# Kernel optimization log

Hardware: AMD Instinct MI355X
Metric: run time of the kernel (lower is better)

The kernel has to match this reference:

```python
import jax, jax.numpy as jnp
import numpy as np

D_MODEL = 512
NUM_HEADS = 8
DEPTH = D_MODEL // NUM_HEADS


def setup_inputs() -> dict:
    key = jax.random.key(0)
    ks = jax.random.split(key, 12)
    B, S, D = 2, 4096, D_MODEL
    scale = 1.0 / np.sqrt(D)
    return {
        "q": jax.random.normal(ks[0], (B, S, D), jnp.float32),
        "k": jax.random.normal(ks[1], (B, S, D), jnp.float32),
        "v": jax.random.normal(ks[2], (B, S, D), jnp.float32),
        "mask": jnp.zeros((B, 1, 1, S), jnp.float32),
        "wq": jax.random.normal(ks[3], (D, D), jnp.float32) * scale,
        "bq": jnp.zeros((D,), jnp.float32),
        "wk": jax.random.normal(ks[4], (D, D), jnp.float32) * scale,
        "bk": jnp.zeros((D,), jnp.float32),
        "wv": jax.random.normal(ks[5], (D, D), jnp.float32) * scale,
        "bv": jnp.zeros((D,), jnp.float32),
        "wo": jax.random.normal(ks[6], (D, D), jnp.float32) * scale,
        "bo": jnp.zeros((D,), jnp.float32),
    }


def _split_heads(x):
    # [B, S, D] -> [B, H, S, depth]
    B, S, _ = x.shape
    return x.reshape(B, S, NUM_HEADS, DEPTH).transpose(0, 2, 1, 3)


def reference(q, k, v, mask, wq, bq, wk, bk, wv, bv, wo, bo):
    B, S, D = q.shape
    query = _split_heads(q @ wq + bq)   # [B,H,S,d]
    key = _split_heads(k @ wk + bk)
    value = _split_heads(v @ wv + bv)
    # NOTE: original module does NOT scale by 1/sqrt(depth)
    score = jnp.einsum("bhqd,bhkd->bhqk", query, key)
    score = score + mask * -1e9
    attn = jax.nn.softmax(score, axis=-1)
    out = jnp.einsum("bhqk,bhkd->bhqd", attn, value)  # [B,H,S,d]
    out = out.transpose(0, 2, 1, 3).reshape(B, S, D)
    return out @ wo + bo
```

## Files before the change

kernel.cpp:

```cpp
#include <hip/hip_runtime.h>

#define NH   8
#define DH   64
#define NB   2
#define SEQ  4096
#define DM   512
#define MR   (NB * SEQ)
#define LSTR 72
#define LOG2E 1.44269504089f
#define NSPL 2
#define KVS  (SEQ / NSPL)
#define RH   (NB * NH * SEQ)
#define PSTR 36

using f16x8 = __attribute__((ext_vector_type(8))) _Float16;
using f32x4 = __attribute__((ext_vector_type(4))) float;
using h2    = __attribute__((ext_vector_type(2))) _Float16;
#define MFMA16(a, b, c) __builtin_amdgcn_mfma_f32_16x16x32_f16(a, b, c, 0, 0, 0)

#if defined(__has_builtin) && __has_builtin(__builtin_amdgcn_exp2f)
#define EXP2(x) __builtin_amdgcn_exp2f(x)
#else
extern "C" __device__ float __ocml_native_exp2_f32(float);
#define EXP2(x) __ocml_native_exp2_f32(x)
#endif

__device__ __forceinline__ unsigned pk_f16(float a, float b) {
    typedef __fp16 fp16v2 __attribute__((ext_vector_type(2)));
    union { fp16v2 h; unsigned u; } c;
    c.h = __builtin_amdgcn_cvt_pkrtz(a, b);
    return c.u;
}
__device__ __forceinline__ float m3(float a, float b, float c) {
    return fmaxf(fmaxf(a, b), c);
}
__device__ __forceinline__ float dot2acc(unsigned u, float c) {
#if defined(__has_builtin) && __has_builtin(__builtin_amdgcn_fdot2)
    h2 a = __builtin_bit_cast(h2, u);
    h2 one = {(_Float16)1.f, (_Float16)1.f};
    return __builtin_amdgcn_fdot2(a, one, c, false);
#else
    h2 a = __builtin_bit_cast(h2, u);
    return c + (float)a[0] + (float)a[1];
#endif
}
__device__ __forceinline__ void async16(void* lds, const void* g) {
    __builtin_amdgcn_global_load_lds(
        (__attribute__((address_space(1))) void*)g,
        (__attribute__((address_space(3))) void*)lds, 16, 0, 0);
}

__global__ __launch_bounds__(256) void cvt_w(
    const float* __restrict__ w0, const float* __restrict__ w1,
    const float* __restrict__ w2, const float* __restrict__ w3,
    _Float16* __restrict__ Wt)
{
    __shared__ _Float16 T[64 * LSTR];
    const int z = blockIdx.z;
    const float* W = (z == 0) ? w0 : (z == 1 ? w1 : (z == 2 ? w2 : w3));
    _Float16* out = Wt + (size_t)z * DM * DM;
    const int t = threadIdx.x;
    const int k0 = blockIdx.x * 64, n0 = blockIdx.y * 64;
#pragma unroll
    for (int i = 0; i < 4; ++i) {
        const int kl  = i * 16 + (t >> 4);
        const int nl4 = (t & 15) * 4;
        float4 u = *(const float4*)(W + (size_t)(k0 + kl) * DM + n0 + nl4);
        T[(nl4 + 0) * LSTR + kl] = (_Float16)u.x;
        T[(nl4 + 1) * LSTR + kl] = (_Float16)u.y;
        T[(nl4 + 2) * LSTR + kl] = (_Float16)u.z;
        T[(nl4 + 3) * LSTR + kl] = (_Float16)u.w;
    }
    __syncthreads();
#pragma unroll
    for (int i = 0; i < 2; ++i) {
        const int nl = i * 32 + (t >> 3);
        const int kc = (t & 7) * 8;
        *(uint4*)(out + (size_t)(n0 + nl) * DM + k0 + kc) = *(const uint4*)&T[nl * LSTR + kc];
    }
}

__global__ __launch_bounds__(256) void maskprep(const float* __restrict__ mask,
                                                float* __restrict__ mw)
{
    const int i = blockIdx.x * 256 + threadIdx.x;
    mw[i] = mask[i] * (-1e9f * LOG2E);
}

__global__ __launch_bounds__(256) void cvt_qkv(
    const float* __restrict__ q, const float* __restrict__ k,
    const float* __restrict__ v,
    _Float16* __restrict__ Qo, _Float16* __restrict__ Ko, _Float16* __restrict__ Vo)
{
    const size_t PER = (size_t)MR * DM;
    size_t base = ((size_t)blockIdx.x * 256 + threadIdx.x) * 8;
    const int tz = (int)(base / PER);
    const size_t off = base % PER;
    const float* s = (tz == 0) ? q : (tz == 1 ? k : v);
    _Float16* d    = (tz == 0) ? Qo : (tz == 1 ? Ko : Vo);
    float4 a = *(const float4*)(s + off);
    float4 b = *(const float4*)(s + off + 4);
    uint4 p = make_uint4(pk_f16(a.x, a.y), pk_f16(a.z, a.w),
                         pk_f16(b.x, b.y), pk_f16(b.z, b.w));
    *(uint4*)(d + off) = p;
}

__global__ __launch_bounds__(256) void proj3(
    const _Float16* __restrict__ Qin, const _Float16* __restrict__ Kin,
    const _Float16* __restrict__ Vin, const _Float16* __restrict__ Wt,
    const float* __restrict__ bq, const float* __restrict__ bk,
    const float* __restrict__ bv,
    _Float16* __restrict__ Qo, _Float16* __restrict__ Ko,
    _Float16* __restrict__ VTo)
{
    __shared__ _Float16 Xs[2][128 * 64];
    __shared__ _Float16 Ws[2][64 * 64];

    const int z = blockIdx.z;
    const _Float16* X = (z == 0) ? Qin : (z == 1 ? Kin : Vin);
    const _Float16* W = Wt + (size_t)z * DM * DM;
    const float* bias = (z == 0) ? bq : (z == 1 ? bk : bv);
    const float scale = (z == 0) ? LOG2E : 1.0f;

    const int t = threadIdx.x;
    const int l = t & 63, w = t >> 6;
    const int m = l & 15, g = l >> 4;
    const int ms = m & 7;
    const int row0 = blockIdx.x * 128;
    const int col0 = blockIdx.y * 64;

    int xr[4], xsw[4];
#pragma unroll
    for (int i = 0; i < 4; ++i) {
        const int c = w * 256 + i * 64 + l;
        xr[i]  = c >> 3;
        xsw[i] = ((c & 7) ^ (xr[i] & 7)) * 8;
    }
    int wr[2], wsw[2];
#pragma unroll
    for (int i = 0; i < 2; ++i) {
        const int c = w * 128 + i * 64 + l;
        wr[i]  = c >> 3;
        wsw[i] = ((c & 7) ^ (wr[i] & 7)) * 8;
    }

#pragma unroll
    for (int i = 0; i < 4; ++i)
        async16(&Xs[0][(w * 256 + i * 64) * 8], X + (size_t)(row0 + xr[i]) * DM + xsw[i]);
#pragma unroll
    for (int i = 0; i < 2; ++i)
        async16(&Ws[0][(w * 128 + i * 64) * 8], W + (size_t)(col0 + wr[i]) * DM + wsw[i]);

    f32x4 acc[2][4] = {};

    for (int k0 = 0; k0 < DM; k0 += 64) {
        const int p = (k0 >> 6) & 1;
        __syncthreads();
        if (k0 + 64 < DM) {
            const int kn = k0 + 64;
#pragma unroll
            for (int i = 0; i < 4; ++i)
                async16(&Xs[p ^ 1][(w * 256 + i * 64) * 8],
                        X + (size_t)(row0 + xr[i]) * DM + kn + xsw[i]);
#pragma unroll
            for (int i = 0; i < 2; ++i)
                async16(&Ws[p ^ 1][(w * 128 + i * 64) * 8],
                        W + (size_t)(col0 + wr[i]) * DM + kn + wsw[i]);
        }
#pragma unroll
        for (int kk = 0; kk < 2; ++kk) {
            const int slot = ((kk * 4 + g) ^ ms) * 8;
            f16x8 a0 = *(const f16x8*)&Xs[p][(w * 32 + m) * 64 + slot];
            f16x8 a1 = *(const f16x8*)&Xs[p][(w * 32 + 16 + m) * 64 + slot];
#pragma unroll
            for (int ct = 0; ct < 4; ++ct) {
                f16x8 bf = *(const f16x8*)&Ws[p][(ct * 16 + m) * 64 + slot];
                acc[0][ct] = MFMA16(a0, bf, acc[0][ct]);
                acc[1][ct] = MFMA16(a1, bf, acc[1][ct]);
            }
        }
    }

    float bv4[4];
#pragma unroll
    for (int ct = 0; ct < 4; ++ct) bv4[ct] = bias[col0 + ct * 16 + m];

    if (z == 2) {
        __syncthreads();
        _Float16* T = &Xs[0][0];
#pragma unroll
        for (int rt = 0; rt < 2; ++rt)
#pragma unroll
            for (int reg = 0; reg < 4; ++reg) {
                const int s_l = w * 32 + rt * 16 + g * 4 + reg;
#pragma unroll
                for (int ct = 0; ct < 4; ++ct) {
                    const int d = ct * 16 + m;
                    T[d * 136 + s_l] = (_Float16)(acc[rt][ct][reg] + bv4[ct]);
                }
            }
        __syncthreads();
        const int bb = row0 >> 12;
        const int s0 = row0 & (SEQ - 1);
#pragma unroll
        for (int j = 0; j < 4; ++j) {
            const int c = j * 256 + t;
            const int d = c >> 4;
            const int sc = (c & 15) * 8;
            *(uint4*)(VTo + (((size_t)bb * NH + blockIdx.y) * DH + d) * SEQ + s0 + sc) =
                *(const uint4*)&T[d * 136 + sc];
        }
    } else {
        _Float16* out = (z == 0) ? Qo : Ko;
#pragma unroll
        for (int rt = 0; rt < 2; ++rt)
#pragma unroll
            for (int reg = 0; reg < 4; ++reg) {
                const int row = row0 + w * 32 + rt * 16 + g * 4 + reg;
                const int bb = row >> 12;
                const int s  = row & (SEQ - 1);
#pragma unroll
                for (int ct = 0; ct < 4; ++ct)
                    out[(((size_t)bb * NH + blockIdx.y) * SEQ + s) * DH + ct * 16 + m] =
                        (_Float16)(scale * (acc[rt][ct][reg] + bv4[ct]));
            }
    }
}

__global__ __launch_bounds__(256) void gemm_out(const _Float16* __restrict__ X,
                                                const _Float16* __restrict__ W,
                                                const float* __restrict__ bias,
                                                float* __restrict__ out)
{
    __shared__ _Float16 Xs[2][128 * 64];
    __shared__ _Float16 Ws[2][64 * 64];

    const int t = threadIdx.x;
    const int l = t & 63, w = t >> 6;
    const int m = l & 15, g = l >> 4;
    const int ms = m & 7;
    const int row0 = blockIdx.x * 128;
    const int col0 = blockIdx.y * 64;

    int xr[4], xsw[4];
#pragma unroll
    for (int i = 0; i < 4; ++i) {
        const int c = w * 256 + i * 64 + l;
        xr[i]  = c >> 3;
        xsw[i] = ((c & 7) ^ (xr[i] & 7)) * 8;
    }
    int wr[2], wsw[2];
#pragma unroll
    for (int i = 0; i < 2; ++i) {
        const int c = w * 128 + i * 64 + l;
        wr[i]  = c >> 3;
        wsw[i] = ((c & 7) ^ (wr[i] & 7)) * 8;
    }

#pragma unroll
    for (int i = 0; i < 4; ++i)
        async16(&Xs[0][(w * 256 + i * 64) * 8], X + (size_t)(row0 + xr[i]) * DM + xsw[i]);
#pragma unroll
    for (int i = 0; i < 2; ++i)
        async16(&Ws[0][(w * 128 + i * 64) * 8], W + (size_t)(col0 + wr[i]) * DM + wsw[i]);

    f32x4 acc[2][4] = {};

    for (int k0 = 0; k0 < DM; k0 += 64) {
        const int p = (k0 >> 6) & 1;
        __syncthreads();
        if (k0 + 64 < DM) {
            const int kn = k0 + 64;
#pragma unroll
            for (int i = 0; i < 4; ++i)
                async16(&Xs[p ^ 1][(w * 256 + i * 64) * 8],
                        X + (size_t)(row0 + xr[i]) * DM + kn + xsw[i]);
#pragma unroll
            for (int i = 0; i < 2; ++i)
                async16(&Ws[p ^ 1][(w * 128 + i * 64) * 8],
                        W + (size_t)(col0 + wr[i]) * DM + kn + wsw[i]);
        }
#pragma unroll
        for (int kk = 0; kk < 2; ++kk) {
            const int slot = ((kk * 4 + g) ^ ms) * 8;
            f16x8 a0 = *(const f16x8*)&Xs[p][(w * 32 + m) * 64 + slot];
            f16x8 a1 = *(const f16x8*)&Xs[p][(w * 32 + 16 + m) * 64 + slot];
#pragma unroll
            for (int ct = 0; ct < 4; ++ct) {
                f16x8 bf = *(const f16x8*)&Ws[p][(ct * 16 + m) * 64 + slot];
                acc[0][ct] = MFMA16(a0, bf, acc[0][ct]);
                acc[1][ct] = MFMA16(a1, bf, acc[1][ct]);
            }
        }
    }

    float bv4[4];
#pragma unroll
    for (int ct = 0; ct < 4; ++ct) bv4[ct] = bias[col0 + ct * 16 + m];

#pragma unroll
    for (int rt = 0; rt < 2; ++rt)
#pragma unroll
        for (int reg = 0; reg < 4; ++reg) {
            const int row = row0 + w * 32 + rt * 16 + g * 4 + reg;
#pragma unroll
            for (int ct = 0; ct < 4; ++ct)
                out[(size_t)row * DM + col0 + ct * 16 + m] = acc[rt][ct][reg] + bv4[ct];
        }
}

__global__ __launch_bounds__(256, 3) void flash_mfma(
    const _Float16* __restrict__ Q, const _Float16* __restrict__ K,
    const _Float16* __restrict__ VT, const float* __restrict__ mw,
    _Float16* __restrict__ Op, float* __restrict__ Ml)
{
    __shared__ _Float16 Ks [2][64 * 64];
    __shared__ _Float16 VTs[2][64 * 64];
    __shared__ unsigned Ps[4][32 * PSTR];

    const int t = threadIdx.x;
    const int l = t & 63, w = t >> 6;
    const int m = l & 15, g = l >> 4;

    const unsigned wfl = blockIdx.x + 32u * blockIdx.y + 512u * blockIdx.z;
    const unsigned o   = (wfl & 7u) * 128u + (wfl >> 3);
    const int q0 = (int)(o & 31u) * 128;
    const int bh = (int)(o >> 5) & 15;
    const int z  = (int)(o >> 9);
    const int b  = bh >> 3;
    const int kb0 = z * KVS;

    const _Float16* Qh  = Q  + (size_t)bh * SEQ * DH;
    const _Float16* Kh  = K  + (size_t)bh * SEQ * DH;
    const _Float16* VTh = VT + (size_t)bh * DH * SEQ;
    const float* mwb = mw + (size_t)b * SEQ;

    const int c0 = w * 128 + l, c1 = c0 + 64;
    const int r0 = c0 >> 3,     r1 = c1 >> 3;
    const int cl0 = (c0 & 7) ^ (r0 & 7), cl1 = (c1 & 7) ^ (r1 & 7);
    const int    gK0 = r0 * DH + cl0 * 8, gK1 = r1 * DH + cl1 * 8;
    const size_t gV0 = (size_t)r0 * SEQ + cl0 * 8, gV1 = (size_t)r1 * SEQ + cl1 * 8;
    const int ldsA = w * 1024, ldsB = ldsA + 512;

    async16(&Ks[0][ldsA], Kh + (size_t)kb0 * DH + gK0);
    async16(&Ks[0][ldsB], Kh + (size_t)kb0 * DH + gK1);
    async16(&VTs[0][ldsA], VTh + kb0 + gV0);
    async16(&VTs[0][ldsB], VTh + kb0 + gV1);

    f16x8 qf[2][2];
#pragma unroll
    for (int h = 0; h < 2; ++h)
#pragma unroll
        for (int kk = 0; kk < 2; ++kk)
            qf[h][kk] = *(const f16x8*)(Qh + (size_t)(q0 + w * 32 + h * 16 + m) * DH +
                                        kk * 32 + g * 8);

    f32x4 mv[4];
#pragma unroll
    for (int kt = 0; kt < 4; ++kt)
        mv[kt] = *(const f32x4*)&mwb[kb0 + kt * 16 + g * 4];

    float m_r[2] = {-INFINITY, -INFINITY}, l_r[2] = {0.f, 0.f};
    f32x4 oacc[2][4] = {};

    unsigned* Pw = &Ps[w][0];
    const int ms = m & 7;

    for (int it = 0; it < KVS / 64; ++it) {
        const int t0 = kb0 + it * 64;
        const int p  = it & 1;
        const bool more = (it + 1 < KVS / 64);
        __syncthreads();

        f32x4 mvn[4];
        if (more) {
            const int tn = t0 + 64;
            async16(&Ks[p ^ 1][ldsA], Kh + (size_t)tn * DH + gK0);
            async16(&Ks[p ^ 1][ldsB], Kh + (size_t)tn * DH + gK1);
            async16(&VTs[p ^ 1][ldsA], VTh + tn + gV0);
            async16(&VTs[p ^ 1][ldsB], VTh + tn + gV1);
#pragma unroll
            for (int kt = 0; kt < 4; ++kt)
                mvn[kt] = *(const f32x4*)&mwb[tn + kt * 16 + g * 4];
        }

        f32x4 sacc[2][4];
#pragma unroll
        for (int kt = 0; kt < 4; ++kt) {
            sacc[0][kt] = mv[kt];
            sacc[1][kt] = mv[kt];
        }
#pragma unroll
        for (int kk = 0; kk < 2; ++kk) {
            const int slot = ((kk * 4 + g) ^ ms) * 8;
#pragma unroll
            for (int kt = 0; kt < 4; ++kt) {
                f16x8 kf = *(const f16x8*)&Ks[p][(kt * 16 + m) * 64 + slot];
                sacc[0][kt] = MFMA16(kf, qf[0][kk], sacc[0][kt]);
                sacc[1][kt] = MFMA16(kf, qf[1][kk], sacc[1][kt]);
            }
        }

        float lmax[2];
#pragma unroll
        for (int h = 0; h < 2; ++h) {
            const float x0 = m3(sacc[h][0][0], sacc[h][0][1], sacc[h][0][2]);
            const float x1 = m3(sacc[h][0][3], sacc[h][1][0], sacc[h][1][1]);
            const float x2 = m3(sacc[h][1][2], sacc[h][1][3], sacc[h][2][0]);
            const float x3 = m3(sacc[h][2][1], sacc[h][2][2], sacc[h][2][3]);
            const float x4 = m3(sacc[h][3][0], sacc[h][3][1], sacc[h][3][2]);
            lmax[h] = fmaxf(m3(x0, x1, x2), m3(x3, x4, sacc[h][3][3]));
        }

        if (!__all(lmax[0] <= m_r[0] + 8.f && lmax[1] <= m_r[1] + 8.f)) {
#pragma unroll
            for (int h = 0; h < 2; ++h) {
                float r = fmaxf(lmax[h], __shfl_xor(lmax[h], 16));
                r = fmaxf(r, __shfl_xor(r, 32));
                const float mnew  = fmaxf(m_r[h], r);
                const float alpha = EXP2(m_r[h] - mnew);
                m_r[h] = mnew;
                l_r[h] *= alpha;
#pragma unroll
                for (int dt = 0; dt < 4; ++dt)
#pragma unroll
                    for (int r4 = 0; r4 < 4; ++r4) oacc[h][dt][r4] *= alpha;
            }
        }

#pragma unroll
        for (int h = 0; h < 2; ++h) {
            const int pwr = (h * 16 + m) * PSTR + g * 2;
            const f32x4 mh = {m_r[h], m_r[h], m_r[h], m_r[h]};
            float ps0 = 0.f, ps1 = 0.f;
#pragma unroll
            for (int kt = 0; kt < 4; ++kt) {
                const f32x4 d = sacc[h][kt] - mh;
                const float p0 = EXP2(d[0]);
                const float p1 = EXP2(d[1]);
                const float p2 = EXP2(d[2]);
                const float p3 = EXP2(d[3]);
                const unsigned u0 = pk_f16(p0, p1);
                const unsigned u1 = pk_f16(p2, p3);
                *(uint2*)&Pw[pwr + kt * 8] = make_uint2(u0, u1);
                if (kt < 2) {
                    ps0 = dot2acc(u0, ps0);
                    ps0 = dot2acc(u1, ps0);
                } else {
                    ps1 = dot2acc(u0, ps1);
                    ps1 = dot2acc(u1, ps1);
                }
            }
            l_r[h] += ps0 + ps1;
        }

#pragma unroll
        for (int kk = 0; kk < 2; ++kk) {
            union { uint4 u4; f16x8 h; } pf[2];
#pragma unroll
            for (int h = 0; h < 2; ++h)
                pf[h].u4 = *(const uint4*)&Pw[(h * 16 + m) * PSTR + kk * 16 + g * 4];
            const int slot = ((kk * 4 + g) ^ ms) * 8;
#pragma unroll
            for (int dt = 0; dt < 4; ++dt) {
                f16x8 vf = *(const f16x8*)&VTs[p][(dt * 16 + m) * 64 + slot];
                oacc[0][dt] = MFMA16(vf, pf[0].h, oacc[0][dt]);
                oacc[1][dt] = MFMA16(vf, pf[1].h, oacc[1][dt]);
            }
        }

        if (more) {
#pragma unroll
            for (int kt = 0; kt < 4; ++kt) mv[kt] = mvn[kt];
        }
    }

#pragma unroll
    for (int h = 0; h < 2; ++h) {
        float lv = l_r[h];
        lv += __shfl_xor(lv, 16);
        lv += __shfl_xor(lv, 32);
        const float inv = 1.0f / lv;
        const int q = q0 + w * 32 + h * 16 + m;
        const size_t rowi = ((size_t)z * NB * NH + bh) * SEQ + q;
        _Float16* Orow = Op + rowi * DH;
#pragma unroll
        for (int dt = 0; dt < 4; ++dt) {
            _Float16 o4[4] = { (_Float16)(oacc[h][dt][0] * inv),
                               (_Float16)(oacc[h][dt][1] * inv),
                               (_Float16)(oacc[h][dt][2] * inv),
                               (_Float16)(oacc[h][dt][3] * inv) };
            *(uint2*)(Orow + dt * 16 + g * 4) = *(const uint2*)o4;
        }
        if (g == 0) ((float2*)Ml)[rowi] = make_float2(m_r[h], lv);
    }
}

__global__ __launch_bounds__(256) void combine(const _Float16* __restrict__ Op,
                                               const float* __restrict__ Ml,
                                               _Float16* __restrict__ O)
{
    const int i = blockIdx.x * 256 + threadIdx.x;
    const int r = i >> 4;
    const int dq = (i & 15) * 4;
    const float2 ml0 = ((const float2*)Ml)[r];
    const float2 ml1 = ((const float2*)Ml)[RH + r];
    const float M = fmaxf(ml0.x, ml1.x);
    float a0 = EXP2(ml0.x - M) * ml0.y;
    float a1 = EXP2(ml1.x - M) * ml1.y;
    const float inv = 1.f / (a0 + a1);
    a0 *= inv; a1 *= inv;
    union { uint2 u; _Float16 h[4]; } v0, v1, o;
    v0.u = *(const uint2*)(Op + (size_t)r * DH + dq);
    v1.u = *(const uint2*)(Op + ((size_t)RH + r) * DH + dq);
#pragma unroll
    for (int j = 0; j < 4; ++j)
        o.h[j] = (_Float16)(a0 * (float)v0.h[j] + a1 * (float)v1.h[j]);
    const int bh = r >> 12, q = r & (SEQ - 1);
    const int b = bh >> 3, h = bh & 7;
    *(uint2*)(O + ((size_t)b * SEQ + q) * DM + h * DH + dq) = o.u;
}

extern "C" void kernel_launch(void* const* d_in, const int* in_sizes, int n_in,
                              void* d_out, int out_size, void* d_ws, size_t ws_size,
                              hipStream_t stream) {
    const float* q    = (const float*)d_in[0];
    const float* k    = (const float*)d_in[1];
    const float* v    = (const float*)d_in[2];
    const float* mask = (const float*)d_in[3];
    const float* wq   = (const float*)d_in[4];
    const float* bq   = (const float*)d_in[5];
    const float* wk   = (const float*)d_in[6];
    const float* bk   = (const float*)d_in[7];
    const float* wv   = (const float*)d_in[8];
    const float* bv   = (const float*)d_in[9];
    const float* wo   = (const float*)d_in[10];
    const float* bo   = (const float*)d_in[11];

    const size_t P8 = (size_t)MR * DM;
    _Float16* Wt  = (_Float16*)d_ws;
    float*    mw  = (float*)(Wt + (size_t)4 * DM * DM);
    _Float16* Qin = (_Float16*)(mw + NB * SEQ);
    _Float16* Kin = Qin + P8;
    _Float16* Vin = Kin + P8;
    _Float16* Qws = Vin + P8;
    _Float16* Kws = Qws + P8;
    _Float16* VTws = Kws + P8;
    _Float16* Ows  = VTws + P8;

    _Float16* Opart = Qin;
    float*    Mlb   = (float*)Vin;

    cvt_w<<<dim3(8, 8, 4), 256, 0, stream>>>(wq, wk, wv, wo, Wt);
    maskprep<<<dim3(NB * SEQ / 256), 256, 0, stream>>>(mask, mw);
    cvt_qkv<<<dim3(3 * (MR * DM / 8) / 256), 256, 0, stream>>>(q, k, v, Qin, Kin, Vin);

    proj3<<<dim3(MR / 128, DM / 64, 3), 256, 0, stream>>>(
        Qin, Kin, Vin, Wt, bq, bk, bv, Qws, Kws, VTws);

    flash_mfma<<<dim3(SEQ / 128, NB * NH, NSPL), 256, 0, stream>>>(
        Qws, Kws, VTws, mw, Opart, Mlb);

    combine<<<dim3(RH * 16 / 256), 256, 0, stream>>>(Opart, Mlb, Ows);

    gemm_out<<<dim3(MR / 128, DM / 64), 256, 0, stream>>>(
        Ows, Wt + (size_t)3 * DM * DM, bo, (float*)d_out);
}
```

Baseline: 250.3 us.

## Split attention KV range into four partitions and combine four partials

Raises the number of KV splits in the flash attention kernel from two to four, doubling the grid size, and remaps block indices accordingly. Partial outputs are stored across reused workspace buffers, and the combine kernel merges four partial results using their max/sum statistics. This aims to improve CU occupancy and wave balance at the cost of more partial-output traffic and a heavier combine pass.

```diff
diff --git a/kernel.cpp b/kernel.cpp
--- a/kernel.cpp
+++ b/kernel.cpp
@@ -8,7 +8,7 @@
 #define MR   (NB * SEQ)
 #define LSTR 72
 #define LOG2E 1.44269504089f
-#define NSPL 2
+#define NSPL 4
 #define KVS  (SEQ / NSPL)
 #define RH   (NB * NH * SEQ)
 #define PSTR 36
@@ -312,7 +312,8 @@
 __global__ __launch_bounds__(256, 3) void flash_mfma(
     const _Float16* __restrict__ Q, const _Float16* __restrict__ K,
     const _Float16* __restrict__ VT, const float* __restrict__ mw,
-    _Float16* __restrict__ Op, float* __restrict__ Ml)
+    _Float16* __restrict__ OpC, _Float16* __restrict__ OpE,
+    float* __restrict__ Ml)
 {
     __shared__ _Float16 Ks [2][64 * 64];
     __shared__ _Float16 VTs[2][64 * 64];
@@ -323,7 +324,7 @@
     const int m = l & 15, g = l >> 4;
 
     const unsigned wfl = blockIdx.x + 32u * blockIdx.y + 512u * blockIdx.z;
-    const unsigned o   = (wfl & 7u) * 128u + (wfl >> 3);
+    const unsigned o   = (wfl & 7u) * 256u + (wfl >> 3);
     const int q0 = (int)(o & 31u) * 128;
     const int bh = (int)(o >> 5) & 15;
     const int z  = (int)(o >> 9);
@@ -334,6 +335,8 @@
     const _Float16* Kh  = K  + (size_t)bh * SEQ * DH;
     const _Float16* VTh = VT + (size_t)bh * DH * SEQ;
     const float* mwb = mw + (size_t)b * SEQ;
+
+    _Float16* Opz = (z < 3) ? (OpC + (size_t)z * RH * DH) : OpE;
 
     const int c0 = w * 128 + l, c1 = c0 + 64;
     const int r0 = c0 >> 3,     r1 = c1 >> 3;
@@ -482,8 +485,8 @@
         lv += __shfl_xor(lv, 32);
         const float inv = 1.0f / lv;
         const int q = q0 + w * 32 + h * 16 + m;
-        const size_t rowi = ((size_t)z * NB * NH + bh) * SEQ + q;
-        _Float16* Orow = Op + rowi * DH;
+        const size_t row = (size_t)bh * SEQ + q;
+        _Float16* Orow = Opz + row * DH;
 #pragma unroll
         for (int dt = 0; dt < 4; ++dt) {
             _Float16 o4[4] = { (_Float16)(oacc[h][dt][0] * inv),
@@ -492,30 +495,42 @@
                                (_Float16)(oacc[h][dt][3] * inv) };
             *(uint2*)(Orow + dt * 16 + g * 4) = *(const uint2*)o4;
         }
-        if (g == 0) ((float2*)Ml)[rowi] = make_float2(m_r[h], lv);
-    }
-}
-
-__global__ __launch_bounds__(256) void combine(const _Float16* __restrict__ Op,
+        if (g == 0) ((float2*)Ml)[(size_t)z * RH + row] = make_float2(m_r[h], lv);
+    }
+}
+
+__global__ __launch_bounds__(256) void combine(const _Float16* __restrict__ OpC,
+                                               const _Float16* __restrict__ OpE,
                                                const float* __restrict__ Ml,
                                                _Float16* __restrict__ O)
 {
     const int i = blockIdx.x * 256 + threadIdx.x;
     const int r = i >> 4;
     const int dq = (i & 15) * 4;
-    const float2 ml0 = ((const float2*)Ml)[r];
-    const float2 ml1 = ((const float2*)Ml)[RH + r];
-    const float M = fmaxf(ml0.x, ml1.x);
-    float a0 = EXP2(ml0.x - M) * ml0.y;
-    float a1 = EXP2(ml1.x - M) * ml1.y;
-    const float inv = 1.f / (a0 + a1);
-    a0 *= inv; a1 *= inv;
-    union { uint2 u; _Float16 h[4]; } v0, v1, o;
-    v0.u = *(const uint2*)(Op + (size_t)r * DH + dq);
-    v1.u = *(const uint2*)(Op + ((size_t)RH + r) * DH + dq);
-#pragma unroll
-    for (int j = 0; j < 4; ++j)
-        o.h[j] = (_Float16)(a0 * (float)v0.h[j] + a1 * (float)v1.h[j]);
+    float2 ml[NSPL];
+#pragma unroll
+    for (int zz = 0; zz < NSPL; ++zz)
+        ml[zz] = ((const float2*)Ml)[(size_t)zz * RH + r];
+    float M = fmaxf(fmaxf(ml[0].x, ml[1].x), fmaxf(ml[2].x, ml[3].x));
+    float a[NSPL], s = 0.f;
+#pragma unroll
+    for (int zz = 0; zz < NSPL; ++zz) {
+        a[zz] = EXP2(ml[zz].x - M) * ml[zz].y;
+        s += a[zz];
+    }
+    const float inv = 1.f / s;
+    float acc4[4] = {0.f, 0.f, 0.f, 0.f};
+#pragma unroll
+    for (int zz = 0; zz < NSPL; ++zz) {
+        const _Float16* base = (zz < 3) ? (OpC + (size_t)zz * RH * DH) : OpE;
+        union { uint2 u; _Float16 h[4]; } v;
+        v.u = *(const uint2*)(base + (size_t)r * DH + dq);
+#pragma unroll
+        for (int j = 0; j < 4; ++j) acc4[j] += a[zz] * (float)v.h[j];
+    }
+    union { uint2 u; _Float16 h[4]; } o;
+#pragma unroll
+    for (int j = 0; j < 4; ++j) o.h[j] = (_Float16)(acc4[j] * inv);
     const int bh = r >> 12, q = r & (SEQ - 1);
     const int b = bh >> 3, h = bh & 7;
     *(uint2*)(O + ((size_t)b * SEQ + q) * DM + h * DH + dq) = o.u;
@@ -546,10 +561,11 @@
     _Float16* Qws = Vin + P8;
     _Float16* Kws = Qws + P8;
     _Float16* VTws = Kws + P8;
-    _Float16* Ows  = VTws + P8;
-
-    _Float16* Opart = Qin;
-    float*    Mlb   = (float*)Vin;
+    _Float16* OpE  = VTws + P8;
+    float*    Mlb  = (float*)(OpE + P8);
+
+    _Float16* OpC  = Qin;
+    _Float16* Ofin = Qws;
 
     cvt_w<<<dim3(8, 8, 4), 256, 0, stream>>>(wq, wk, wv, wo, Wt);
     maskprep<<<dim3(NB * SEQ / 256), 256, 0, stream>>>(mask, mw);
@@ -559,10 +575,10 @@
         Qin, Kin, Vin, Wt, bq, bk, bv, Qws, Kws, VTws);
 
     flash_mfma<<<dim3(SEQ / 128, NB * NH, NSPL), 256, 0, stream>>>(
-        Qws, Kws, VTws, mw, Opart, Mlb);
-
-    combine<<<dim3(RH * 16 / 256), 256, 0, stream>>>(Opart, Mlb, Ows);
+        Qws, Kws, VTws, mw, OpC, OpE, Mlb);
+
+    combine<<<dim3(RH * 16 / 256), 256, 0, stream>>>(OpC, OpE, Mlb, Ofin);
 
     gemm_out<<<dim3(MR / 128, DM / 64), 256, 0, stream>>>(
-        Ows, Wt + (size_t)3 * DM * DM, bo, (float*)d_out);
-}
+        Ofin, Wt + (size_t)3 * DM * DM, bo, (float*)d_out);
+}
```

Result: no change. 254.5 us (+1.7%).
